# Optimization experiments

Hardware: AMD Instinct MI355X
Metric: run time of the kernel (lower is better)

Reference implementation:

```python
import jax, jax.numpy as jnp
import numpy as np

T, B = 50, 8192
ACTION_DIM, STATE_DIM, LATENT_DIM, HIDDEN_DIM = 6, 200, 30, 200


def _linear_params(key, out_f, in_f):
    k1, k2 = jax.random.split(key)
    bound = 1.0 / np.sqrt(in_f)
    W = jax.random.uniform(k1, (out_f, in_f), jnp.float32, -bound, bound)
    b = jax.random.uniform(k2, (out_f,), jnp.float32, -bound, bound)
    return W, b


def setup_inputs() -> dict:
    key = jax.random.key(0)
    ks = jax.random.split(key, 10)
    actions = jax.random.normal(ks[0], (T, B, ACTION_DIM), jnp.float32)
    h = jnp.zeros((B, STATE_DIM), jnp.float32)
    s = jnp.zeros((B, LATENT_DIM), jnp.float32)
    noise = jax.random.normal(ks[1], (T, B, LATENT_DIM), jnp.float32)
    W_fc, b_fc = _linear_params(ks[2], STATE_DIM, LATENT_DIM + ACTION_DIM)
    # torch GRUCell: weight_ih [3*H, In], weight_hh [3*H, H], gate order (r, z, n)
    W_ih, b_ih = _linear_params(ks[3], 3 * STATE_DIM, STATE_DIM)
    W_hh, b_hh = _linear_params(ks[4], 3 * STATE_DIM, STATE_DIM)
    W1, b1 = _linear_params(ks[5], HIDDEN_DIM, STATE_DIM)
    Wmu, bmu = _linear_params(ks[6], LATENT_DIM, HIDDEN_DIM)
    Wvar, bvar = _linear_params(ks[7], LATENT_DIM, HIDDEN_DIM)
    return {"actions": actions, "h": h, "s": s, "noise": noise,
            "W_fc": W_fc, "b_fc": b_fc, "W_ih": W_ih, "b_ih": b_ih,
            "W_hh": W_hh, "b_hh": b_hh, "W1": W1, "b1": b1,
            "Wmu": Wmu, "bmu": bmu, "Wvar": Wvar, "bvar": bvar}


def reference(actions, h, s, noise, W_fc, b_fc, W_ih, b_ih, W_hh, b_hh,
              W1, b1, Wmu, bmu, Wvar, bvar):
    H = STATE_DIM

    def step(carry, inp):
        h, s = carry
        a, eps = inp
        # deterministic_fc: concat(s, a) -> state_dim
        x = jnp.concatenate([s, a], axis=-1) @ W_fc.T + b_fc
        # GRUCell
        gi = x @ W_ih.T + b_ih  # [B, 3H]
        gh = h @ W_hh.T + b_hh
        r = jax.nn.sigmoid(gi[:, :H] + gh[:, :H])
        z = jax.nn.sigmoid(gi[:, H:2 * H] + gh[:, H:2 * H])
        n = jnp.tanh(gi[:, 2 * H:] + r * gh[:, 2 * H:])
        h_new = (1.0 - z) * n + z * h
        # prior_latent (NormalLinear)
        hid = jax.nn.relu(h_new @ W1.T + b1)
        mu = hid @ Wmu.T + bmu
        var = jax.nn.softplus(hid @ Wvar.T + bvar) + 0.1
        # torch.distributions.Normal(mu, var): second arg is SCALE
        s_new = mu + var * eps
        return (h_new, s_new), (h_new, s_new)

    (_, _), (states, stoch_states) = jax.lax.scan(step, (h, s), (actions, noise))
    return states, stoch_states
```

## Files before the change

kernel.cpp:

```cpp
#include <hip/hip_runtime.h>
#include <hip/hip_bf16.h>
#include <cmath>

#define T_STEPS 50
#define BATCH   8192
#define ROWS    32
#define NBLK    (BATCH / ROWS)
#define THREADS 512

typedef float  f32x4  __attribute__((ext_vector_type(4)));
typedef __bf16 bf16x8 __attribute__((ext_vector_type(8)));
typedef unsigned int u32x4 __attribute__((ext_vector_type(4)));
typedef unsigned short u16x4 __attribute__((ext_vector_type(4)));

#define N_R9   (13*9*512)
#define N_NI   (13*2*512)
#define N_NH   (13*7*512)
#define N_W1   (13*7*512)
#define N_MV   (4*7*512)
#define OFF_R  0
#define OFF_Z  (OFF_R  + N_R9)
#define OFF_NI (OFF_Z  + N_R9)
#define OFF_NH (OFF_NI + N_NI)
#define OFF_W1 (OFF_NH + N_NH)
#define OFF_MV (OFF_W1 + N_W1)
#define W_TOTAL (OFF_MV + N_MV)

__device__ __forceinline__ unsigned short f2b(float f) {
    union { float f; unsigned u; } v; v.f = f;
    unsigned r = v.u + 0x7FFFu + ((v.u >> 16) & 1u);
    return (unsigned short)(r >> 16);
}
__device__ __forceinline__ float b2f(unsigned short h) {
    union { unsigned u; float f; } v; v.u = ((unsigned)h) << 16;
    return v.f;
}
__device__ __forceinline__ int fragSlot(int row, int k) {
    int sub = k & 31;
    return ((((sub >> 3) & 3) << 4) | row) * 8 + (sub & 7);
}
__device__ __forceinline__ f32x4 MFMA(bf16x8 a, bf16x8 b, f32x4 c) {
    return __builtin_amdgcn_mfma_f32_16x16x32_bf16(a, b, c, 0, 0, 0);
}
__device__ __forceinline__ float fast_rcp(float x) { return __builtin_amdgcn_rcpf(x); }
__device__ __forceinline__ float sigmf(float x) {
    return fast_rcp(1.f + __expf(-x));
}
__device__ __forceinline__ float tanh_fast(float x) {
    float e = __expf(2.f * fminf(x, 40.f));
    return (e - 1.f) * fast_rcp(e + 1.f);
}
__device__ __forceinline__ void st_nt4(float* p, f32x4 v) {
    __builtin_nontemporal_store(v, reinterpret_cast<f32x4*>(p));
}
__device__ __forceinline__ float ld_nt(const float* p) { return __builtin_nontemporal_load(p); }

__global__ void rssm_prep(const float* __restrict__ Wfc, const float* __restrict__ Wih,
                          const float* __restrict__ Whh, const float* __restrict__ W1,
                          const float* __restrict__ Wmu, const float* __restrict__ Wvar,
                          unsigned short* __restrict__ out)
{
    int idx = blockIdx.x * 256 + threadIdx.x;
    if (idx >= W_TOTAL) return;
    float v = 0.f;
    if (idx < OFF_NI) {
        const int base = (idx < OFF_Z) ? OFF_R : OFF_Z;
        const int grow = (idx < OFF_Z) ? 0 : 200;
        int loc = idx - base;
        int nt = loc / (9 * 512), r = loc % (9 * 512), ks = r / 512, li = r % 512;
        int lane = li >> 3, e = li & 7;
        int n = nt * 16 + (lane & 15);
        int k = ks * 32 + (lane >> 4) * 8 + e;
        if (n < 200) {
            if (k < 36) {
                float acc = 0.f;
                for (int m = 0; m < 200; ++m)
                    acc += Wih[(grow + n) * 200 + m] * Wfc[m * 36 + k];
                v = acc;
            } else if (k >= 64 && (k - 64) < 200) {
                v = Whh[(grow + n) * 200 + (k - 64)];
            }
        }
    } else if (idx < OFF_NH) {
        int loc = idx - OFF_NI;
        int nt = loc / (2 * 512), r = loc % (2 * 512), ks = r / 512, li = r % 512;
        int lane = li >> 3, e = li & 7;
        int n = nt * 16 + (lane & 15);
        int k = ks * 32 + (lane >> 4) * 8 + e;
        if (n < 200 && k < 36) {
            float acc = 0.f;
            for (int m = 0; m < 200; ++m)
                acc += Wih[(400 + n) * 200 + m] * Wfc[m * 36 + k];
            v = acc;
        }
    } else if (idx < OFF_W1) {
        int loc = idx - OFF_NH;
        int nt = loc / (7 * 512), r = loc % (7 * 512), ks = r / 512, li = r % 512;
        int lane = li >> 3, e = li & 7;
        int n = nt * 16 + (lane & 15);
        int k = ks * 32 + (lane >> 4) * 8 + e;
        if (n < 200 && k < 200) v = Whh[(400 + n) * 200 + k];
    } else if (idx < OFF_MV) {
        int loc = idx - OFF_W1;
        int nt = loc / (7 * 512), r = loc % (7 * 512), ks = r / 512, li = r % 512;
        int lane = li >> 3, e = li & 7;
        int n = nt * 16 + (lane & 15);
        int k = ks * 32 + (lane >> 4) * 8 + e;
        if (n < 200 && k < 200) v = W1[n * 200 + k];
    } else {
        int loc = idx - OFF_MV;
        int nt = loc / (7 * 512), r = loc % (7 * 512), ks = r / 512, li = r % 512;
        int lane = li >> 3, e = li & 7;
        int k = ks * 32 + (lane >> 4) * 8 + e;
        if (nt < 2) { int m = nt * 16 + (lane & 15); if (m < 30 && k < 200) v = Wmu[m * 200 + k]; }
        else        { int m = (nt - 2) * 16 + (lane & 15); if (m < 30 && k < 200) v = Wvar[m * 200 + k]; }
    }
    out[idx] = f2b(v);
}

__global__ void rssm_bias(const float* __restrict__ Wih, const float* __restrict__ b_fc,
                          const float* __restrict__ b_ih, const float* __restrict__ b_hh,
                          float* __restrict__ cb)
{
    int j = blockIdx.x * 64 + threadIdx.x;
    if (j >= 624) return;
    int g = j / 208, n = j % 208;
    float v = 0.f;
    if (n < 200) {
        float acc = 0.f;
        for (int m = 0; m < 200; ++m)
            acc += Wih[(g * 200 + n) * 200 + m] * b_fc[m];
        if (g == 0)      v = acc + b_ih[n] + b_hh[n];
        else if (g == 1) v = acc + b_ih[200 + n] + b_hh[200 + n];
        else             v = acc + b_ih[400 + n];
    }
    cb[g * 208 + n] = v;
}

__global__ __launch_bounds__(THREADS, 2) void rssm_main(
    const float* __restrict__ actions, const float* __restrict__ h0,
    const float* __restrict__ s0, const float* __restrict__ noise,
    const float* __restrict__ b_hh, const float* __restrict__ b1,
    const float* __restrict__ bmu, const float* __restrict__ bvar,
    const unsigned short* __restrict__ W, float* __restrict__ out)
{
    __shared__ __align__(16) unsigned short Hb[2][2 * 7 * 512];
    __shared__ __align__(16) unsigned short HIDb[2 * 7 * 512];
    __shared__ __align__(16) unsigned short SAb[2 * 2 * 512];
    __shared__ __align__(16) unsigned short STG_S[ROWS * 200];
    __shared__ __align__(16) float STG_Z[ROWS * 30];
    __shared__ __align__(16) float NZb[ROWS * 30];
    __shared__ __align__(16) unsigned short W1L[N_W1];

    const int tid = threadIdx.x;
    const int w = tid >> 6, lane = tid & 63;
    const int col = lane & 15, kg = lane >> 4;
    const int brow0 = blockIdx.x * ROWS;
    const int jt0 = w;
    const int jt1 = (w < 5) ? (w + 8) : -1;

    const unsigned short* WR  = W + OFF_R;
    const unsigned short* WZ  = W + OFF_Z;
    const unsigned short* WNI = W + OFF_NI;
    const unsigned short* WNH = W + OFF_NH;
    const unsigned short* W1w = W + OFF_W1;
    const unsigned short* WMV = W + OFF_MV;
    const float* CB = (const float*)(W + W_TOTAL);
    float* out_states = out;
    float* out_stoch  = out + (size_t)T_STEPS * BATCH * 200;

    float brv[2] = {0.f, 0.f}, bzv[2] = {0.f, 0.f}, biv[2] = {0.f, 0.f};
    float bhv[2] = {0.f, 0.f}, b1v[2] = {0.f, 0.f};
    #pragma unroll
    for (int ji = 0; ji < 2; ++ji) {
        const int jt = ji ? jt1 : jt0;
        if (jt < 0) continue;
        const int j = jt * 16 + col;
        if (j < 200) {
            brv[ji] = CB[j];
            bzv[ji] = CB[208 + j];
            biv[ji] = CB[416 + j];
            bhv[ji] = b_hh[400 + j];
            b1v[ji] = b1[j];
        }
    }
    float bmuv = 0.f, bvav = 0.f;
    if (w < 4) {
        const int jm = (w & 1) * 16 + col;
        if (jm < 30) { bmuv = bmu[jm]; bvav = bvar[jm]; }
    }

    for (int i = tid; i < 2 * 7 * 512; i += THREADS) { Hb[0][i] = 0; Hb[1][i] = 0; }
    for (int i = tid; i < 2 * 7 * 512; i += THREADS) HIDb[i] = 0;
    for (int i = tid; i < 2 * 2 * 512; i += THREADS) SAb[i] = 0;
    {
        const u32x4* s1 = reinterpret_cast<const u32x4*>(W1w);
        u32x4* d1 = reinterpret_cast<u32x4*>(W1L);
        for (int i = tid; i < N_W1 / 8; i += THREADS) d1[i] = s1[i];
    }
    __syncthreads();
    for (int i = tid; i < ROWS * 200; i += THREADS) {
        int r = i / 200, jj = i % 200;
        Hb[0][((r >> 4) * 7 + (jj >> 5)) * 512 + fragSlot(r & 15, jj)] =
            f2b(h0[(size_t)(brow0 + r) * 200 + jj]);
    }
    for (int i = tid; i < ROWS * 30; i += THREADS) {
        int r = i / 30, jj = i % 30;
        SAb[((r >> 4) * 2) * 512 + fragSlot(r & 15, jj)] =
            f2b(s0[(size_t)(brow0 + r) * 30 + jj]);
    }
    for (int i = tid; i < ROWS * 6; i += THREADS) {
        int r = i / 6, c = i % 6, k = 30 + c;
        SAb[((r >> 4) * 2 + (k >> 5)) * 512 + fragSlot(r & 15, k)] =
            f2b(ld_nt(&actions[(size_t)(brow0 + r) * 6 + c]));
    }
    __syncthreads();

    for (int t = 0; t < T_STEPS; ++t) {
        const int cur = t & 1, nxt = cur ^ 1;

        #pragma unroll
        for (int ji = 0; ji < 2; ++ji) {
            const int jt = ji ? jt1 : jt0;
            if (jt < 0) continue;
            bf16x8 wRr[9], wZr[9], wNi[2], wNh[7];
            #pragma unroll
            for (int ks = 0; ks < 9; ++ks) {
                wRr[ks] = *reinterpret_cast<const bf16x8*>(&WR[(size_t)(jt * 9 + ks) * 512 + lane * 8]);
                wZr[ks] = *reinterpret_cast<const bf16x8*>(&WZ[(size_t)(jt * 9 + ks) * 512 + lane * 8]);
            }
            #pragma unroll
            for (int ks = 0; ks < 2; ++ks)
                wNi[ks] = *reinterpret_cast<const bf16x8*>(&WNI[(size_t)(jt * 2 + ks) * 512 + lane * 8]);
            #pragma unroll
            for (int ks = 0; ks < 7; ++ks)
                wNh[ks] = *reinterpret_cast<const bf16x8*>(&WNH[(size_t)(jt * 7 + ks) * 512 + lane * 8]);

            f32x4 aR[2], aZ[2], aNi[2], aNh[2];
            #pragma unroll
            for (int mt = 0; mt < 2; ++mt) {
                aR[mt]  = (f32x4){brv[ji], brv[ji], brv[ji], brv[ji]};
                aZ[mt]  = (f32x4){bzv[ji], bzv[ji], bzv[ji], bzv[ji]};
                aNi[mt] = (f32x4){biv[ji], biv[ji], biv[ji], biv[ji]};
                aNh[mt] = (f32x4){bhv[ji], bhv[ji], bhv[ji], bhv[ji]};
            }
            #pragma unroll
            for (int ks = 0; ks < 9; ++ks) {
                #pragma unroll
                for (int mt = 0; mt < 2; ++mt) {
                    bf16x8 a = (ks < 2)
                        ? *reinterpret_cast<const bf16x8*>(&SAb[(mt * 2 + ks) * 512 + lane * 8])
                        : *reinterpret_cast<const bf16x8*>(&Hb[cur][(mt * 7 + (ks - 2)) * 512 + lane * 8]);
                    aR[mt] = MFMA(a, wRr[ks], aR[mt]);
                    aZ[mt] = MFMA(a, wZr[ks], aZ[mt]);
                    if (ks < 2) aNi[mt] = MFMA(a, wNi[ks], aNi[mt]);
                    else        aNh[mt] = MFMA(a, wNh[ks - 2], aNh[mt]);
                }
            }
            const int j = jt * 16 + col;
            const bool jv = (j < 200);
            #pragma unroll
            for (int mt = 0; mt < 2; ++mt) {
                #pragma unroll
                for (int q = 0; q < 4; ++q) {
                    const int r0 = kg * 4 + q;
                    const int slot = (j >> 5) * 512 + fragSlot(r0, j);
                    float rg = sigmf(aR[mt][q]);
                    float zg = sigmf(aZ[mt][q]);
                    float ng = tanh_fast(aNi[mt][q] + rg * aNh[mt][q]);
                    if (jv) {
                        float hv = b2f(Hb[cur][mt * 7 * 512 + slot]);
                        float hn = ng + zg * (hv - ng);
                        unsigned short hb = f2b(hn);
                        Hb[nxt][mt * 7 * 512 + slot] = hb;
                        STG_S[(mt * 16 + r0) * 200 + j] = hb;
                    }
                }
            }
        }
        if (jt1 < 0) {
            const int idx = (w - 5) * 64 + lane;
            const float* np = noise + ((size_t)t * BATCH + brow0) * 30;
            for (int i = idx; i < ROWS * 30; i += 192)
                NZb[i] = ld_nt(&np[i]);
            if (t >= 1) {
                float* dst = out_stoch + ((size_t)(t - 1) * BATCH + brow0) * 30;
                for (int i = idx; i < 240; i += 192) {
                    f32x4 v = *reinterpret_cast<const f32x4*>(&STG_Z[i * 4]);
                    st_nt4(dst + i * 4, v);
                }
            }
        }
        __syncthreads();

        #pragma unroll
        for (int ji = 0; ji < 2; ++ji) {
            const int jt = ji ? jt1 : jt0;
            if (jt < 0) continue;
            f32x4 c0 = {b1v[ji], b1v[ji], b1v[ji], b1v[ji]};
            f32x4 c1 = {b1v[ji], b1v[ji], b1v[ji], b1v[ji]};
            #pragma unroll
            for (int ks = 0; ks < 7; ++ks) {
                bf16x8 wbv = *reinterpret_cast<const bf16x8*>(&W1L[(size_t)(jt * 7 + ks) * 512 + lane * 8]);
                bf16x8 a0 = *reinterpret_cast<const bf16x8*>(&Hb[nxt][(0 * 7 + ks) * 512 + lane * 8]);
                bf16x8 a1 = *reinterpret_cast<const bf16x8*>(&Hb[nxt][(1 * 7 + ks) * 512 + lane * 8]);
                c0 = MFMA(a0, wbv, c0);
                c1 = MFMA(a1, wbv, c1);
            }
            const int j = jt * 16 + col;
            #pragma unroll
            for (int q = 0; q < 4; ++q) {
                HIDb[(0 * 7 + (j >> 5)) * 512 + fragSlot(kg * 4 + q, j)] = f2b(fmaxf(c0[q], 0.f));
                HIDb[(1 * 7 + (j >> 5)) * 512 + fragSlot(kg * 4 + q, j)] = f2b(fmaxf(c1[q], 0.f));
            }
        }
        __syncthreads();

        if (w < 4) {
            const int mt = w >> 1, ntile = w & 1;
            bf16x8 wm[7], wv[7];
            #pragma unroll
            for (int ks = 0; ks < 7; ++ks) {
                wm[ks] = *reinterpret_cast<const bf16x8*>(&WMV[(size_t)(ntile * 7 + ks) * 512 + lane * 8]);
                wv[ks] = *reinterpret_cast<const bf16x8*>(&WMV[(size_t)((2 + ntile) * 7 + ks) * 512 + lane * 8]);
            }
            f32x4 cm = {bmuv, bmuv, bmuv, bmuv};
            f32x4 cv = {bvav, bvav, bvav, bvav};
            #pragma unroll
            for (int ks = 0; ks < 7; ++ks) {
                bf16x8 a = *reinterpret_cast<const bf16x8*>(&HIDb[(mt * 7 + ks) * 512 + lane * 8]);
                cm = MFMA(a, wm[ks], cm);
                cv = MFMA(a, wv[ks], cv);
            }
            const int jm = ntile * 16 + col;
            const bool jmv = (jm < 30);
            #pragma unroll
            for (int q = 0; q < 4; ++q) {
                const int r0 = kg * 4 + q;
                const int row = mt * 16 + r0;
                float mu = cm[q];
                float vr = cv[q];
                float var = ((vr > 20.f) ? vr : log1pf(__expf(vr))) + 0.1f;
                if (jmv) {
                    float eps = NZb[row * 30 + jm];
                    float sn = mu + var * eps;
                    STG_Z[row * 30 + jm] = sn;
                    SAb[(mt * 2) * 512 + fragSlot(r0, jm)] = f2b(sn);
                }
            }
        } else {
            const int di = (w - 4) * 64 + lane;
            float* dst = out_states + ((size_t)t * BATCH + brow0) * 200;
            for (int i = di; i < 1600; i += 256) {
                u16x4 hv4 = *reinterpret_cast<const u16x4*>(&STG_S[i * 4]);
                f32x4 v;
                v[0] = b2f(hv4[0]); v[1] = b2f(hv4[1]);
                v[2] = b2f(hv4[2]); v[3] = b2f(hv4[3]);
                st_nt4(dst + i * 4, v);
            }
            if (t + 1 < T_STEPS && di < ROWS * 6) {
                const int r = di / 6, c = di % 6, k = 30 + c;
                float av = ld_nt(&actions[((size_t)(t + 1) * BATCH + brow0 + r) * 6 + c]);
                SAb[((r >> 4) * 2 + (k >> 5)) * 512 + fragSlot(r & 15, k)] = f2b(av);
            }
        }
        __syncthreads();
    }

    if (tid < 240) {
        f32x4 v = *reinterpret_cast<const f32x4*>(&STG_Z[tid * 4]);
        st_nt4(out_stoch + ((size_t)(T_STEPS - 1) * BATCH + brow0) * 30 + tid * 4, v);
    }
}

extern "C" void kernel_launch(void* const* d_in, const int* in_sizes, int n_in,
                              void* d_out, int out_size, void* d_ws, size_t ws_size,
                              hipStream_t stream)
{
    const float* actions = (const float*)d_in[0];
    const float* h0      = (const float*)d_in[1];
    const float* s0      = (const float*)d_in[2];
    const float* noise   = (const float*)d_in[3];
    const float* Wfc     = (const float*)d_in[4];
    const float* bfc     = (const float*)d_in[5];
    const float* Wih     = (const float*)d_in[6];
    const float* bih     = (const float*)d_in[7];
    const float* Whh     = (const float*)d_in[8];
    const float* bhh     = (const float*)d_in[9];
    const float* W1      = (const float*)d_in[10];
    const float* b1      = (const float*)d_in[11];
    const float* Wmu     = (const float*)d_in[12];
    const float* bmu     = (const float*)d_in[13];
    const float* Wvar    = (const float*)d_in[14];
    const float* bvar    = (const float*)d_in[15];

    unsigned short* wbuf = (unsigned short*)d_ws;
    float* cb = (float*)(wbuf + W_TOTAL);

    rssm_prep<<<(W_TOTAL + 255) / 256, 256, 0, stream>>>(Wfc, Wih, Whh, W1, Wmu, Wvar, wbuf);
    rssm_bias<<<10, 64, 0, stream>>>(Wih, bfc, bih, bhh, cb);
    rssm_main<<<NBLK, THREADS, 0, stream>>>(actions, h0, s0, noise, bhh, b1,
                                            bmu, bvar, wbuf, (float*)d_out);
}
```

Baseline: 775.3 us.

## Write hidden states from double-buffered H one step late, drop STG_S staging

Removes the STG_S shared staging buffer and the per-element duplicate store into it. The three idle warps (w>=5) now write the previous step's hidden state straight from the Hb double buffer at the start of each step, which overlaps with the GRU MFMA work. It also moves the noise prefetch to the start of the step. This frees shared memory and takes the state store off the phase-2 warps, at the cost of more work for the idle warps and a final epilogue store. The reads rely on the fragSlot layout putting 4 consecutive j values contiguously.

```diff
diff --git a/kernel.cpp b/kernel.cpp
--- a/kernel.cpp
+++ b/kernel.cpp
@@ -147,7 +147,6 @@
     __shared__ __align__(16) unsigned short Hb[2][2 * 7 * 512];
     __shared__ __align__(16) unsigned short HIDb[2 * 7 * 512];
     __shared__ __align__(16) unsigned short SAb[2 * 2 * 512];
-    __shared__ __align__(16) unsigned short STG_S[ROWS * 200];
     __shared__ __align__(16) float STG_Z[ROWS * 30];
     __shared__ __align__(16) float NZb[ROWS * 30];
     __shared__ __align__(16) unsigned short W1L[N_W1];
@@ -219,6 +218,31 @@
     for (int t = 0; t < T_STEPS; ++t) {
         const int cur = t & 1, nxt = cur ^ 1;
 
+        if (jt1 < 0) {
+            const int idx = (w - 5) * 64 + lane;
+            if (t >= 1) {
+                float* dstz = out_stoch + ((size_t)(t - 1) * BATCH + brow0) * 30;
+                for (int i = idx; i < 240; i += 192) {
+                    f32x4 v = *reinterpret_cast<const f32x4*>(&STG_Z[i * 4]);
+                    st_nt4(dstz + i * 4, v);
+                }
+                float* dsts = out_states + ((size_t)(t - 1) * BATCH + brow0) * 200;
+                for (int i = idx; i < 1600; i += 192) {
+                    const int e0 = i * 4;
+                    const int r = e0 / 200, j0 = e0 % 200;
+                    const int mt = r >> 4, rr = r & 15;
+                    u16x4 hv4 = *reinterpret_cast<const u16x4*>(
+                        &Hb[cur][(mt * 7 + (j0 >> 5)) * 512 + fragSlot(rr, j0)]);
+                    f32x4 v;
+                    v[0] = b2f(hv4[0]); v[1] = b2f(hv4[1]);
+                    v[2] = b2f(hv4[2]); v[3] = b2f(hv4[3]);
+                    st_nt4(dsts + e0, v);
+                }
+            }
+            const float* np = noise + ((size_t)t * BATCH + brow0) * 30;
+            for (int i = idx; i < ROWS * 30; i += 192)
+                NZb[i] = ld_nt(&np[i]);
+        }
         #pragma unroll
         for (int ji = 0; ji < 2; ++ji) {
             const int jt = ji ? jt1 : jt0;
@@ -271,23 +295,8 @@
                     if (jv) {
                         float hv = b2f(Hb[cur][mt * 7 * 512 + slot]);
                         float hn = ng + zg * (hv - ng);
-                        unsigned short hb = f2b(hn);
-                        Hb[nxt][mt * 7 * 512 + slot] = hb;
-                        STG_S[(mt * 16 + r0) * 200 + j] = hb;
+                        Hb[nxt][mt * 7 * 512 + slot] = f2b(hn);
                     }
-                }
-            }
-        }
-        if (jt1 < 0) {
-            const int idx = (w - 5) * 64 + lane;
-            const float* np = noise + ((size_t)t * BATCH + brow0) * 30;
-            for (int i = idx; i < ROWS * 30; i += 192)
-                NZb[i] = ld_nt(&np[i]);
-            if (t >= 1) {
-                float* dst = out_stoch + ((size_t)(t - 1) * BATCH + brow0) * 30;
-                for (int i = idx; i < 240; i += 192) {
-                    f32x4 v = *reinterpret_cast<const f32x4*>(&STG_Z[i * 4]);
-                    st_nt4(dst + i * 4, v);
                 }
             }
         }
@@ -350,14 +359,6 @@
             }
         } else {
             const int di = (w - 4) * 64 + lane;
-            float* dst = out_states + ((size_t)t * BATCH + brow0) * 200;
-            for (int i = di; i < 1600; i += 256) {
-                u16x4 hv4 = *reinterpret_cast<const u16x4*>(&STG_S[i * 4]);
-                f32x4 v;
-                v[0] = b2f(hv4[0]); v[1] = b2f(hv4[1]);
-                v[2] = b2f(hv4[2]); v[3] = b2f(hv4[3]);
-                st_nt4(dst + i * 4, v);
-            }
             if (t + 1 < T_STEPS && di < ROWS * 6) {
                 const int r = di / 6, c = di % 6, k = 30 + c;
                 float av = ld_nt(&actions[((size_t)(t + 1) * BATCH + brow0 + r) * 6 + c]);
@@ -367,9 +368,24 @@
         __syncthreads();
     }
 
-    if (tid < 240) {
-        f32x4 v = *reinterpret_cast<const f32x4*>(&STG_Z[tid * 4]);
-        st_nt4(out_stoch + ((size_t)(T_STEPS - 1) * BATCH + brow0) * 30 + tid * 4, v);
+    {
+        const int fin = T_STEPS & 1;
+        float* dsts = out_states + ((size_t)(T_STEPS - 1) * BATCH + brow0) * 200;
+        for (int i = tid; i < 1600; i += THREADS) {
+            const int e0 = i * 4;
+            const int r = e0 / 200, j0 = e0 % 200;
+            const int mt = r >> 4, rr = r & 15;
+            u16x4 hv4 = *reinterpret_cast<const u16x4*>(
+                &Hb[fin][(mt * 7 + (j0 >> 5)) * 512 + fragSlot(rr, j0)]);
+            f32x4 v;
+            v[0] = b2f(hv4[0]); v[1] = b2f(hv4[1]);
+            v[2] = b2f(hv4[2]); v[3] = b2f(hv4[3]);
+            st_nt4(dsts + e0, v);
+        }
+        if (tid < 240) {
+            f32x4 v = *reinterpret_cast<const f32x4*>(&STG_Z[tid * 4]);
+            st_nt4(out_stoch + ((size_t)(T_STEPS - 1) * BATCH + brow0) * 30 + tid * 4, v);
+        }
     }
 }
 
```

After: 682.9 us (median of 2 runs). -11.9%, faster.
